# Optimization experiments

Measured on AMD Instinct MI355X. Metric: run time of the kernel, lower is better.

The kernel has to match this reference:

```python
import jax, jax.numpy as jnp
import numpy as np

EPS = 1e-5        # layer_norm_epsilon
N_HEAD = 16
PAD = 50257       # pad_token_id in select_at_last_token
L = 2             # len(layer_nums)


def _ln(x, g, b):
    m = jnp.mean(x, axis=-1, keepdims=True)
    v = jnp.mean(jnp.square(x - m), axis=-1, keepdims=True)
    return (x - m) * jax.lax.rsqrt(v + EPS) * g + b


def _attn_layer(hs, idx, g, b, Wq, Wk, Wv, Wo, bo):
    # hs: [B,S,D]; idx: [B] index of last non-pad token
    B, S, D = hs.shape
    hd = D // N_HEAD
    h = _ln(hs, g, b)
    last = h[jnp.arange(B), idx]                       # [B,D] select_at_last_token
    q = (last @ Wq).reshape(B, N_HEAD, hd)             # single query per sequence
    k = (h @ Wk).reshape(B, S, N_HEAD, hd)
    v = (h @ Wv).reshape(B, S, N_HEAD, hd)
    # GPT-Neo attention: NO 1/sqrt(head_dim) scaling; causal mask for the last
    # row (q_len=1, key_len=S) is all-ones so it is a no-op.
    scores = jnp.einsum('bhd,bshd->bhs', q, k)
    w = jax.nn.softmax(scores, axis=-1)
    o = jnp.einsum('bhs,bshd->bhd', w, v).reshape(B, D)
    return o @ Wo + bo


def setup_inputs() -> dict:
    key = jax.random.key(0)
    ks = jax.random.split(key, 12)
    B, S, D = 8, 2048, 2048
    Dc = L * D            # 4096, MLP input size
    I = 4 * Dc            # 16384, mlp_ratio * Dc
    s = 0.02
    return {
        'hs0': jax.random.normal(ks[0], (B, S, D), jnp.float32),
        'hs1': jax.random.normal(ks[1], (B, S, D), jnp.float32),
        'ids': jax.random.randint(ks[2], (B, S), 0, 50258),
        'ln_g': jnp.ones((L, D), jnp.float32),
        'ln_b': jnp.zeros((L, D), jnp.float32),
        'Wq': jax.random.normal(ks[3], (L, D, D), jnp.float32) * s,
        'Wk': jax.random.normal(ks[4], (L, D, D), jnp.float32) * s,
        'Wv': jax.random.normal(ks[5], (L, D, D), jnp.float32) * s,
        'Wo': jax.random.normal(ks[6], (L, D, D), jnp.float32) * s,
        'bo': jnp.zeros((L, D), jnp.float32),
        'W1': jax.random.normal(ks[7], (Dc, I), jnp.float32) * s,
        'b1': jnp.zeros((I,), jnp.float32),
        'W2': jax.random.normal(ks[8], (I, Dc), jnp.float32) * s,
        'b2': jnp.zeros((Dc,), jnp.float32),
        'Wl': jax.random.normal(ks[9], (Dc, 2), jnp.float32) * s,
        'bl': jnp.zeros((2,), jnp.float32),
    }


def reference(hs0, hs1, ids, ln_g, ln_b, Wq, Wk, Wv, Wo, bo, W1, b1, W2, b2, Wl, bl):
    # select_at_last_token index: argmax of cumsum of non-pad mask = last non-pad pos
    mask = (ids != PAD).astype(jnp.int32)
    idx = jnp.argmax(jnp.cumsum(mask, axis=1), axis=1)  # [B]
    hss = [hs0, hs1]
    attn_outs = [
        _attn_layer(hss[l], idx, ln_g[l], ln_b[l], Wq[l], Wk[l], Wv[l], Wo[l], bo[l])
        for l in range(L)
    ]
    h = jnp.concatenate(attn_outs, axis=-1)            # [B, L*D]
    m = jax.nn.gelu(h @ W1 + b1, approximate=False) @ W2 + b2
    h = h + m                                           # residual around MLP
    return h @ Wl + bl                                  # [B, 2] logits
```

## Files before the change

### kernel.cpp

```cpp
#include <hip/hip_runtime.h>
#include <math.h>

#define PAD_ID 50257
#define B_ 8
#define S_ 2048
#define D_ 2048
#define H_ 16
#define HD_ 128
#define L_ 2
#define DC_ 4096
#define I_ 16384
#define EPS_ 1e-5f

__device__ __forceinline__ int rfl(int x){ return __builtin_amdgcn_readfirstlane(x); }

__global__ __launch_bounds__(256) void kA(const int* __restrict__ ids, int* __restrict__ idx){
  int b = blockIdx.x, t = threadIdx.x;
  __shared__ int red[256];
  int best = -1;
  for (int s = t; s < S_; s += 256)
    if (ids[b*S_+s] != PAD_ID) best = s;
  red[t] = best; __syncthreads();
  for (int off=128; off; off>>=1){ if (t<off) red[t] = max(red[t], red[t+off]); __syncthreads(); }
  if (t==0) idx[b] = max(red[0], 0);
}

__global__ __launch_bounds__(256) void kA2(const float* __restrict__ hs0, const float* __restrict__ hs1,
                    const int* __restrict__ idx,
                    const float* __restrict__ g, const float* __restrict__ bt,
                    float* __restrict__ lnlT){
  int b = blockIdx.x, l = blockIdx.y, t = threadIdx.x;
  const float* hs = (l==0?hs0:hs1);
  const float* row = hs + ((size_t)b*S_ + idx[b])*D_;
  int d0 = t*8;
  float x[8]; float s=0.f, ss=0.f;
  #pragma unroll
  for(int k=0;k<8;k++){ x[k]=row[d0+k]; s+=x[k]; ss+=x[k]*x[k]; }
  __shared__ float r1[256], r2[256];
  r1[t]=s; r2[t]=ss; __syncthreads();
  for(int off=128; off; off>>=1){ if(t<off){ r1[t]+=r1[t+off]; r2[t]+=r2[t+off]; } __syncthreads(); }
  float m = r1[0]*(1.0f/D_); float var = r2[0]*(1.0f/D_) - m*m;
  float rstd = rsqrtf(var + EPS_);
  #pragma unroll
  for(int k=0;k<8;k++){
    int d = d0+k;
    lnlT[((size_t)l*D_ + d)*8 + b] = (x[k]-m)*rstd*g[l*D_+d] + bt[l*D_+d];
  }
}

__global__ __launch_bounds__(256) void gemv8(
    const float* __restrict__ W, const float* __restrict__ Xt, float* __restrict__ outAcc,
    int C, int N, int cs, long wStride, long xStride, long oStride){
  int t = threadIdx.x;
  int l = blockIdx.z;
  W += (size_t)l*wStride; Xt += (size_t)l*xStride; outAcc += (size_t)l*oStride;
  int lane = t & 63;
  int w = rfl(t >> 6);
  int cpw = C/(cs*4);
  int c0 = (blockIdx.y*4 + w)*cpw;
  float acc[8] = {0,0,0,0,0,0,0,0};
  const float* xp = Xt + (size_t)c0*8;
  const float* wp = W + (size_t)c0*N + (size_t)blockIdx.x*64 + lane;
  #pragma unroll 4
  for (int c=0; c<cpw; c++){
    float wv = wp[(size_t)c*N];
    #pragma unroll
    for(int r=0;r<8;r++) acc[r] += xp[c*8+r]*wv;
  }
  __shared__ float red[4][64][8];
  #pragma unroll
  for(int r=0;r<8;r++) red[w][lane][r] = acc[r];
  __syncthreads();
  if (t < 64){
    #pragma unroll
    for(int r=0;r<8;r++){
      float s = red[0][t][r]+red[1][t][r]+red[2][t][r]+red[3][t][r];
      atomicAdd(&outAcc[((size_t)blockIdx.x*64 + t)*8 + r], s);
    }
  }
}

__global__ __launch_bounds__(256) void kC(
    const float* __restrict__ Wk, const float* __restrict__ qT,
    const float* __restrict__ g, const float* __restrict__ bt,
    float* __restrict__ gqk, float* __restrict__ Sg, float* __restrict__ Sb){
  int t = threadIdx.x;
  int dq = blockIdx.x; int h = blockIdx.y; int l = blockIdx.z;
  const float* wkB = Wk + (size_t)l*D_*D_ + h*HD_;
  const float* qB  = qT + ((size_t)l*D_ + h*HD_)*8;
  float sgl[8]={0,0,0,0,0,0,0,0}, sbl[8]={0,0,0,0,0,0,0,0};
  for (int rr=0; rr<2; rr++){
    int dp = dq*512 + rr*256 + t;
    const float* wr = wkB + (size_t)dp*D_;
    float a[8]={0,0,0,0,0,0,0,0};
    #pragma unroll 4
    for (int j=0;j<HD_;j++){
      float wv = wr[j];
      #pragma unroll
      for(int r=0;r<8;r++) a[r] += wv*qB[j*8+r];
    }
    float gg = g[l*D_+dp], bb = bt[l*D_+dp];
    #pragma unroll
    for(int r=0;r<8;r++){
      float gq = gg*a[r];
      gqk[((size_t)(l*8+r)*H_ + h)*D_ + dp] = gq;
      sgl[r] += gq;
      sbl[r] += bb*a[r];
    }
  }
  __shared__ float red[256][8];
  #pragma unroll
  for(int r=0;r<8;r++) red[t][r]=sgl[r];
  __syncthreads();
  for(int off=128; off; off>>=1){ if(t<off){ for(int r=0;r<8;r++) red[t][r]+=red[t+off][r]; } __syncthreads(); }
  if (t<8) atomicAdd(&Sg[(l*8+t)*H_ + h], red[0][t]);
  __syncthreads();
  #pragma unroll
  for(int r=0;r<8;r++) red[t][r]=sbl[r];
  __syncthreads();
  for(int off=128; off; off>>=1){ if(t<off){ for(int r=0;r<8;r++) red[t][r]+=red[t+off][r]; } __syncthreads(); }
  if (t<8) atomicAdd(&Sb[(l*8+t)*H_ + h], red[0][t]);
}

__global__ __launch_bounds__(256) void kD(
    const float* __restrict__ hs0, const float* __restrict__ hs1,
    const float* __restrict__ gqk, const float* __restrict__ Sg, const float* __restrict__ Sb,
    float* __restrict__ scores, float* __restrict__ mu, float* __restrict__ rs){
  int t = threadIdx.x;
  int sc = blockIdx.x, b = blockIdx.y, l = blockIdx.z;
  const float* hs = (l==0?hs0:hs1) + (size_t)b*S_*D_;
  int r = t & 63;
  int jq = rfl(t >> 6);
  int s0 = sc*64;
  __shared__ float lds[64*65];
  float acc[16];
  #pragma unroll
  for(int h=0;h<16;h++) acc[h]=0.f;
  float sum=0.f, sq=0.f;
  const float* gq = gqk + (size_t)(l*8+b)*H_*D_;
  for (int jt=0; jt<32; jt++){
    int jb = jt*64;
    #pragma unroll
    for (int q=0;q<4;q++){
      int fid = t + q*256;
      int row = fid >> 4, jo = (fid & 15)*4;
      const float4 v = *(const float4*)(hs + (size_t)(s0+row)*D_ + jb + jo);
      float* lp = &lds[row*65 + jo];
      lp[0]=v.x; lp[1]=v.y; lp[2]=v.z; lp[3]=v.w;
    }
    __syncthreads();
    #pragma unroll
    for (int jj4=0; jj4<4; jj4++){
      int j = jq*16 + jj4*4;
      float x0 = lds[r*65+j], x1 = lds[r*65+j+1], x2 = lds[r*65+j+2], x3 = lds[r*65+j+3];
      sum += x0+x1+x2+x3;
      sq += x0*x0; sq += x1*x1; sq += x2*x2; sq += x3*x3;
      int jg = jb + j;
      #pragma unroll
      for(int h=0;h<16;h++){
        const float4 gv = *(const float4*)(gq + (size_t)h*D_ + jg);
        acc[h] += x0*gv.x + x1*gv.y + x2*gv.z + x3*gv.w;
      }
    }
    __syncthreads();
  }
  if (jq > 0){
    float* p = &lds[((jq-1)*64 + r)*18];
    #pragma unroll
    for(int h=0;h<16;h++) p[h]=acc[h];
    p[16]=sum; p[17]=sq;
  }
  __syncthreads();
  if (jq == 0){
    #pragma unroll
    for(int g3=0; g3<3; g3++){
      const float* p = &lds[(g3*64 + r)*18];
      #pragma unroll
      for(int h=0;h<16;h++) acc[h]+=p[h];
      sum += p[16]; sq += p[17];
    }
    float m = sum * (1.0f/D_);
    float var = sq * (1.0f/D_) - m*m;
    float rst = rsqrtf(var + EPS_);
    int s = s0 + r;
    int lb = l*8+b;
    mu[(size_t)lb*S_ + s] = m;
    rs[(size_t)lb*S_ + s] = rst;
    #pragma unroll
    for(int h=0;h<16;h++){
      float sgv = Sg[lb*H_ + h], sbv = Sb[lb*H_ + h];
      scores[((size_t)lb*H_ + h)*S_ + s] = rst*(acc[h] - m*sgv) + sbv;
    }
  }
}

__global__ __launch_bounds__(256) void kE1(
    const float* __restrict__ scores, const float* __restrict__ mu, const float* __restrict__ rs,
    float* __restrict__ M, float* __restrict__ Sden, float* __restrict__ cc){
  int t=threadIdx.x; int h=blockIdx.x, b=blockIdx.y, l=blockIdx.z;
  int lb = l*8+b;
  const float* sc = scores + ((size_t)lb*H_ + h)*S_;
  __shared__ float red[256];
  __shared__ float red2[256];
  float mx = -1e30f;
  for (int s=t; s<S_; s+=256) mx = fmaxf(mx, sc[s]);
  red[t]=mx; __syncthreads();
  for(int off=128;off;off>>=1){ if(t<off) red[t]=fmaxf(red[t],red[t+off]); __syncthreads(); }
  float Mv = red[0];
  __syncthreads();
  float se=0.f, sce=0.f;
  const float* mup = mu + (size_t)lb*S_;
  const float* rsp = rs + (size_t)lb*S_;
  for (int s=t; s<S_; s+=256){
    float e = __expf(sc[s]-Mv);
    se += e;
    sce += e*rsp[s]*mup[s];
  }
  red[t]=se; red2[t]=sce; __syncthreads();
  for(int off=128;off;off>>=1){ if(t<off){red[t]+=red[t+off]; red2[t]+=red2[t+off];} __syncthreads(); }
  if(t==0){ M[lb*H_+h]=Mv; Sden[lb*H_+h]=red[0]; cc[lb*H_+h]=red2[0]/red[0]; }
}

__global__ __launch_bounds__(256) void kE2(
    const float* __restrict__ scores, const float* __restrict__ rs,
    const float* __restrict__ M, const float* __restrict__ Sden,
    float* __restrict__ u){
  int t=threadIdx.x; int scb=blockIdx.x, b=blockIdx.y, l=blockIdx.z;
  int lb=l*8+b;
  int lin0 = t*8;
  int sl = lin0 >> 4;
  int h0 = lin0 & 15;
  int s = scb*128 + sl;
  float rstv = rs[(size_t)lb*S_ + s];
  float out[8];
  #pragma unroll
  for(int k=0;k<8;k++){
    int h = h0 + k;
    float e = __expf(scores[((size_t)lb*H_+h)*S_ + s] - M[lb*H_+h]);
    out[k] = e / Sden[lb*H_+h] * rstv;
  }
  float* up = u + ((size_t)lb*S_ + s)*H_ + h0;
  *(float4*)up     = make_float4(out[0],out[1],out[2],out[3]);
  *(float4*)(up+4) = make_float4(out[4],out[5],out[6],out[7]);
}

__global__ __launch_bounds__(256) void kF(
    const float* __restrict__ hs0, const float* __restrict__ hs1,
    const float* __restrict__ u, float* __restrict__ Fpart){
  int t=threadIdx.x;
  int sc = blockIdx.x>>1, dh = blockIdx.x&1;
  int b=blockIdx.y, l=blockIdx.z;
  int lb=l*8+b;
  const float* hs = (l==0?hs0:hs1) + (size_t)b*S_*D_;
  int d0 = dh*1024 + t*4;
  float acc[16][4];
  #pragma unroll
  for(int h=0;h<16;h++){
    #pragma unroll
    for(int k=0;k<4;k++) acc[h][k]=0.f;
  }
  int s0 = sc*128;
  for (int si=0; si<128; si++){
    int s = s0+si;
    const float* up = u + ((size_t)lb*S_ + s)*H_;
    float4 u0 = *(const float4*)up, u1 = *(const float4*)(up+4),
           u2 = *(const float4*)(up+8), u3 = *(const float4*)(up+12);
    float uu[16] = {u0.x,u0.y,u0.z,u0.w, u1.x,u1.y,u1.z,u1.w,
                    u2.x,u2.y,u2.z,u2.w, u3.x,u3.y,u3.z,u3.w};
    float4 x = *(const float4*)(hs + (size_t)s*D_ + d0);
    float xx[4]={x.x,x.y,x.z,x.w};
    #pragma unroll
    for(int h=0;h<16;h++){
      #pragma unroll
      for(int k=0;k<4;k++) acc[h][k] += uu[h]*xx[k];
    }
  }
  #pragma unroll
  for(int h=0;h<16;h++){
    float4 v = make_float4(acc[h][0],acc[h][1],acc[h][2],acc[h][3]);
    *(float4*)(Fpart + (((size_t)lb*16 + sc)*H_ + h)*D_ + d0) = v;
  }
}

__global__ __launch_bounds__(256) void kF2(
    const float* __restrict__ Fpart, const float* __restrict__ g, float* __restrict__ gAT){
  int n = blockIdx.x*256 + threadIdx.x;
  int d = n & (D_-1);
  int h = (n >> 11) & 15;
  int l = n >> 15;
  float gg = g[l*D_+d];
  float out[8];
  #pragma unroll
  for(int b=0;b<8;b++){
    float s=0.f;
    for(int scn=0;scn<16;scn++)
      s += Fpart[(((size_t)(l*8+b)*16 + scn)*H_ + h)*D_ + d];
    out[b]=gg*s;
  }
  float* op = gAT + (size_t)n*8;
  *(float4*)op     = make_float4(out[0],out[1],out[2],out[3]);
  *(float4*)(op+4) = make_float4(out[4],out[5],out[6],out[7]);
}

__global__ __launch_bounds__(256) void kG(
    const float* __restrict__ Wv, const float* __restrict__ gAT,
    const float* __restrict__ g, const float* __restrict__ bt,
    float* __restrict__ Opart){
  int t=threadIdx.x;
  int d4=blockIdx.x, h=blockIdx.y, l=blockIdx.z;
  int j = t & 127;
  int dg = rfl(t >> 7);
  const float* wv = Wv + (size_t)l*D_*D_ + h*HD_ + j;
  const float* gA = gAT + ((size_t)l*H_ + h)*D_*8;
  float acc[8]={0,0,0,0,0,0,0,0}; float ag=0.f, ab=0.f;
  int dstart = d4*512 + dg*256;
  #pragma unroll 2
  for (int dd=0; dd<256; dd++){
    int d = dstart+dd;
    float wvv = wv[(size_t)d*D_];
    const float* xa = gA + (size_t)d*8;
    #pragma unroll
    for(int r=0;r<8;r++) acc[r] += xa[r]*wvv;
    ag += g[l*D_+d]*wvv;
    ab += bt[l*D_+d]*wvv;
  }
  __shared__ float red[2][128][10];
  float* p = red[dg][j];
  #pragma unroll
  for(int r=0;r<8;r++) p[r]=acc[r];
  p[8]=ag; p[9]=ab;
  __syncthreads();
  if (t<128){
    const float* q0=red[0][t]; const float* q1=red[1][t];
    #pragma unroll
    for(int r=0;r<10;r++)
      atomicAdd(&Opart[(((size_t)l*H_+h)*HD_ + t)*10 + r], q0[r]+q1[r]);
  }
}

__global__ __launch_bounds__(256) void kG2(const float* __restrict__ Opart, const float* __restrict__ cc,
                    float* __restrict__ oT){
  int n = blockIdx.x*256 + threadIdx.x;
  int j = n & 127; int h = (n>>7) & 15; int l = n>>11;
  const float* p = Opart + (size_t)n*10;
  float ag=p[8], ab=p[9];
  #pragma unroll
  for(int b=0;b<8;b++){
    float c = cc[(l*8+b)*H_+h];
    oT[((size_t)l*D_ + h*HD_ + j)*8 + b] = p[b] - c*ag + ab;
  }
}

__global__ void kInitH(const float* __restrict__ bo, float* __restrict__ hcatT){
  int n = blockIdx.x*256 + threadIdx.x;
  hcatT[n] = bo[n>>3];
}

__global__ void kH2(float* __restrict__ t1T, const float* __restrict__ b1){
  int i = blockIdx.x*256 + threadIdx.x;
  float bv = b1[i];
  float* p = t1T + (size_t)i*8;
  #pragma unroll
  for(int k=0;k<8;k++){
    float x = p[k] + bv;
    p[k] = 0.5f*x*(1.0f + erff(x*0.70710678118654752440f));
  }
}

__global__ void kH2b(const float* __restrict__ hcatT, const float* __restrict__ b2, float* __restrict__ h2T){
  int j = blockIdx.x*256 + threadIdx.x;
  float bv = b2[j];
  #pragma unroll
  for(int k=0;k<8;k++) h2T[(size_t)j*8+k] = hcatT[(size_t)j*8+k] + bv;
}

__global__ __launch_bounds__(256) void kH4(const float* __restrict__ h2T, const float* __restrict__ Wl,
                    const float* __restrict__ bl, float* __restrict__ out){
  int t=threadIdx.x;
  float acc[8][2];
  #pragma unroll
  for(int b=0;b<8;b++){acc[b][0]=0.f;acc[b][1]=0.f;}
  for (int j=t; j<DC_; j+=256){
    float w0=Wl[j*2], w1=Wl[j*2+1];
    const float* hp = h2T + (size_t)j*8;
    #pragma unroll
    for(int b=0;b<8;b++){ float x=hp[b]; acc[b][0]+=x*w0; acc[b][1]+=x*w1; }
  }
  __shared__ float red[256][16];
  #pragma unroll
  for(int b=0;b<8;b++){ red[t][b*2]=acc[b][0]; red[t][b*2+1]=acc[b][1]; }
  __syncthreads();
  for(int off=128;off;off>>=1){ if(t<off){ for(int k=0;k<16;k++) red[t][k]+=red[t+off][k]; } __syncthreads(); }
  if (t<16) out[t] = red[0][t] + bl[t&1];
}

extern "C" void kernel_launch(void* const* d_in, const int* in_sizes, int n_in,
                              void* d_out, int out_size, void* d_ws, size_t ws_size,
                              hipStream_t stream) {
  (void)in_sizes; (void)n_in; (void)out_size;
  const float* hs0 = (const float*)d_in[0];
  const float* hs1 = (const float*)d_in[1];
  const int*   ids = (const int*)d_in[2];
  const float* ln_g = (const float*)d_in[3];
  const float* ln_b = (const float*)d_in[4];
  const float* Wq = (const float*)d_in[5];
  const float* Wk = (const float*)d_in[6];
  const float* Wv = (const float*)d_in[7];
  const float* Wo = (const float*)d_in[8];
  const float* bo = (const float*)d_in[9];
  const float* W1 = (const float*)d_in[10];
  const float* b1 = (const float*)d_in[11];
  const float* W2 = (const float*)d_in[12];
  const float* b2 = (const float*)d_in[13];
  const float* Wl = (const float*)d_in[14];
  const float* bl = (const float*)d_in[15];
  float* out = (float*)d_out;
  float* ws = (float*)d_ws;

  size_t o = 0;
  int* idx = (int*)ws;        o += 16;
  float* qT = ws + o;         o += (size_t)L_*D_*8;
  float* Sg = ws + o;         o += 256;
  float* Sb = ws + o;         o += 256;
  float* Opart = ws + o;      o += (size_t)L_*H_*HD_*10;
  float* t1T = ws + o;        o += (size_t)I_*8;
  size_t atomicFloats = o - 16;
  float* lnlT = ws + o;       o += (size_t)L_*D_*8;
  float* gqk = ws + o;        o += (size_t)L_*8*H_*D_;
  float* mu = ws + o;         o += (size_t)L_*8*S_;
  float* rs_ = ws + o;        o += (size_t)L_*8*S_;
  float* scores = ws + o;     o += (size_t)L_*8*H_*S_;
  float* M = ws + o;          o += 256;
  float* Sden = ws + o;       o += 256;
  float* cc = ws + o;         o += 256;
  float* u = ws + o;          o += (size_t)L_*8*S_*H_;
  float* Fpart = ws + o;      o += (size_t)L_*8*16*H_*D_;
  float* gAT = ws + o;        o += (size_t)L_*H_*D_*8;
  float* oT = ws + o;         o += (size_t)L_*D_*8;
  float* hcatT = ws + o;      o += (size_t)DC_*8;
  float* h2T = ws + o;        o += (size_t)DC_*8;
  if (o*4 > ws_size) return;

  hipMemsetAsync((void*)(ws + 16), 0, atomicFloats*4, stream);

  kA<<<8,256,0,stream>>>(ids, idx);
  kA2<<<dim3(8,2),256,0,stream>>>(hs0,hs1,idx,ln_g,ln_b,lnlT);
  gemv8<<<dim3(32,2,2),256,0,stream>>>(Wq, lnlT, qT, D_, D_, 2,
                                       (long)D_*D_, (long)D_*8, (long)D_*8);
  kC<<<dim3(4,16,2),256,0,stream>>>(Wk, qT, ln_g, ln_b, gqk, Sg, Sb);
  kD<<<dim3(32,8,2),256,0,stream>>>(hs0,hs1,gqk,Sg,Sb,scores,mu,rs_);
  kE1<<<dim3(16,8,2),256,0,stream>>>(scores,mu,rs_,M,Sden,cc);
  kE2<<<dim3(16,8,2),256,0,stream>>>(scores,rs_,M,Sden,u);
  kF<<<dim3(32,8,2),256,0,stream>>>(hs0,hs1,u,Fpart);
  kF2<<<256,256,0,stream>>>(Fpart, ln_g, gAT);
  kG<<<dim3(4,16,2),256,0,stream>>>(Wv, gAT, ln_g, ln_b, Opart);
  kG2<<<16,256,0,stream>>>(Opart, cc, oT);
  kInitH<<<128,256,0,stream>>>(bo, hcatT);
  gemv8<<<dim3(32,2,2),256,0,stream>>>(Wo, oT, hcatT, D_, D_, 2,
                                       (long)D_*D_, (long)D_*8, (long)D_*8);
  gemv8<<<dim3(256,2,1),256,0,stream>>>(W1, hcatT, t1T, DC_, I_, 2, 0,0,0);
  kH2<<<64,256,0,stream>>>(t1T, b1);
  kH2b<<<16,256,0,stream>>>(hcatT, b2, h2T);
  gemv8<<<dim3(64,8,1),256,0,stream>>>(W2, t1T, h2T, I_, DC_, 8, 0,0,0);
  kH4<<<1,256,0,stream>>>(h2T, Wl, bl, out);
}
```

Measured before the change: 1.134 ms.

## Retile score kernel with LDS-staged gqk, split-K, and widen grids across kernels

The score kernel kD now stages both hs and the gqk tile in LDS and uses a 4-row by 4-column register tile per thread. It splits the D reduction into two halves, then adds a new kD2 kernel that sums the partials and applies the LayerNorm correction. kC, kF, kG and the gemv8 launches are re-split into more blocks with smaller per-thread work to raise parallelism. The change adds an extra kernel launch and a partial-buffer round trip, and it reuses the Fpart workspace for the kD partials.

```diff
diff --git a/kernel.cpp b/kernel.cpp
--- a/kernel.cpp
+++ b/kernel.cpp
@@ -85,28 +85,27 @@
     const float* __restrict__ g, const float* __restrict__ bt,
     float* __restrict__ gqk, float* __restrict__ Sg, float* __restrict__ Sb){
   int t = threadIdx.x;
-  int dq = blockIdx.x; int h = blockIdx.y; int l = blockIdx.z;
-  const float* wkB = Wk + (size_t)l*D_*D_ + h*HD_;
-  const float* qB  = qT + ((size_t)l*D_ + h*HD_)*8;
-  float sgl[8]={0,0,0,0,0,0,0,0}, sbl[8]={0,0,0,0,0,0,0,0};
-  for (int rr=0; rr<2; rr++){
-    int dp = dq*512 + rr*256 + t;
-    const float* wr = wkB + (size_t)dp*D_;
-    float a[8]={0,0,0,0,0,0,0,0};
-    #pragma unroll 4
-    for (int j=0;j<HD_;j++){
-      float wv = wr[j];
-      #pragma unroll
-      for(int r=0;r<8;r++) a[r] += wv*qB[j*8+r];
-    }
-    float gg = g[l*D_+dp], bb = bt[l*D_+dp];
-    #pragma unroll
-    for(int r=0;r<8;r++){
-      float gq = gg*a[r];
-      gqk[((size_t)(l*8+r)*H_ + h)*D_ + dp] = gq;
-      sgl[r] += gq;
-      sbl[r] += bb*a[r];
-    }
+  int h = blockIdx.y; int l = blockIdx.z;
+  int dp = blockIdx.x*256 + t;
+  const float* wr = Wk + (size_t)l*D_*D_ + (size_t)dp*D_ + h*HD_;
+  const float* qB = qT + ((size_t)l*D_ + h*HD_)*8;
+  float a[8]={0,0,0,0,0,0,0,0};
+  #pragma unroll 4
+  for (int j4=0;j4<32;j4++){
+    float4 wv = *(const float4*)(wr + j4*4);
+    const float* qp = qB + j4*32;
+    #pragma unroll
+    for(int r=0;r<8;r++)
+      a[r] += wv.x*qp[r] + wv.y*qp[8+r] + wv.z*qp[16+r] + wv.w*qp[24+r];
+  }
+  float gg = g[l*D_+dp], bb = bt[l*D_+dp];
+  float sgl[8], sbl[8];
+  #pragma unroll
+  for(int r=0;r<8;r++){
+    float gq = gg*a[r];
+    gqk[((size_t)(l*8+r)*H_ + h)*D_ + dp] = gq;
+    sgl[r] = gq;
+    sbl[r] = bb*a[r];
   }
   __shared__ float red[256][8];
   #pragma unroll
@@ -124,73 +123,132 @@
 
 __global__ __launch_bounds__(256) void kD(
     const float* __restrict__ hs0, const float* __restrict__ hs1,
-    const float* __restrict__ gqk, const float* __restrict__ Sg, const float* __restrict__ Sb,
-    float* __restrict__ scores, float* __restrict__ mu, float* __restrict__ rs){
+    const float* __restrict__ gqk,
+    float* __restrict__ accP, float* __restrict__ sumP, float* __restrict__ sqP){
   int t = threadIdx.x;
-  int sc = blockIdx.x, b = blockIdx.y, l = blockIdx.z;
+  int sc = blockIdx.x & 31, kh = blockIdx.x >> 5;
+  int b = blockIdx.y, l = blockIdx.z;
+  int lb = l*8 + b;
   const float* hs = (l==0?hs0:hs1) + (size_t)b*S_*D_;
-  int r = t & 63;
-  int jq = rfl(t >> 6);
+  const float* gqp = gqk + (size_t)lb*H_*D_;
   int s0 = sc*64;
-  __shared__ float lds[64*65];
-  float acc[16];
-  #pragma unroll
-  for(int h=0;h<16;h++) acc[h]=0.f;
-  float sum=0.f, sq=0.f;
-  const float* gq = gqk + (size_t)(l*8+b)*H_*D_;
-  for (int jt=0; jt<32; jt++){
-    int jb = jt*64;
+  int kb = kh*1024;
+  __shared__ float smem[64*66 + 16*68];
+  float* xT = smem;
+  float* gT = smem + 64*66;
+  int rq = t & 15, jg = t >> 4;
+  int r0 = rq*4, jc = jg*4;
+  float acc[4][16];
+  #pragma unroll
+  for(int rr=0;rr<4;rr++){
+    #pragma unroll
+    for(int h=0;h<16;h++) acc[rr][h]=0.f;
+  }
+  float sum[4]={0.f,0.f,0.f,0.f}, sq[4]={0.f,0.f,0.f,0.f};
+  for (int c=0;c<16;c++){
+    int cb = kb + c*64;
     #pragma unroll
     for (int q=0;q<4;q++){
       int fid = t + q*256;
       int row = fid >> 4, jo = (fid & 15)*4;
-      const float4 v = *(const float4*)(hs + (size_t)(s0+row)*D_ + jb + jo);
-      float* lp = &lds[row*65 + jo];
-      lp[0]=v.x; lp[1]=v.y; lp[2]=v.z; lp[3]=v.w;
+      float4 v = *(const float4*)(hs + (size_t)(s0+row)*D_ + cb + jo);
+      float2* wp = (float2*)&xT[row*66 + jo];
+      wp[0] = make_float2(v.x, v.y);
+      wp[1] = make_float2(v.z, v.w);
+    }
+    {
+      int hh = t >> 4, jo = (t & 15)*4;
+      float4 gv = *(const float4*)(gqp + (size_t)hh*D_ + cb + jo);
+      *(float4*)&gT[hh*68 + jo] = gv;
     }
     __syncthreads();
-    #pragma unroll
-    for (int jj4=0; jj4<4; jj4++){
-      int j = jq*16 + jj4*4;
-      float x0 = lds[r*65+j], x1 = lds[r*65+j+1], x2 = lds[r*65+j+2], x3 = lds[r*65+j+3];
-      sum += x0+x1+x2+x3;
-      sq += x0*x0; sq += x1*x1; sq += x2*x2; sq += x3*x3;
-      int jg = jb + j;
+    float xv[4][4];
+    #pragma unroll
+    for (int rr=0;rr<4;rr++){
+      const float2* xp = (const float2*)&xT[(r0+rr)*66 + jc];
+      float2 xa = xp[0], xb = xp[1];
+      xv[rr][0]=xa.x; xv[rr][1]=xa.y; xv[rr][2]=xb.x; xv[rr][3]=xb.y;
+      sum[rr] += xa.x + xa.y + xb.x + xb.y;
+      sq[rr]  += xa.x*xa.x + xa.y*xa.y + xb.x*xb.x + xb.y*xb.y;
+    }
+    #pragma unroll
+    for (int h=0;h<16;h++){
+      float4 gv = *(const float4*)&gT[h*68 + jc];
       #pragma unroll
-      for(int h=0;h<16;h++){
-        const float4 gv = *(const float4*)(gq + (size_t)h*D_ + jg);
-        acc[h] += x0*gv.x + x1*gv.y + x2*gv.z + x3*gv.w;
-      }
+      for (int rr=0;rr<4;rr++)
+        acc[rr][h] += xv[rr][0]*gv.x + xv[rr][1]*gv.y + xv[rr][2]*gv.z + xv[rr][3]*gv.w;
     }
     __syncthreads();
   }
-  if (jq > 0){
-    float* p = &lds[((jq-1)*64 + r)*18];
-    #pragma unroll
-    for(int h=0;h<16;h++) p[h]=acc[h];
-    p[16]=sum; p[17]=sq;
-  }
-  __syncthreads();
-  if (jq == 0){
-    #pragma unroll
-    for(int g3=0; g3<3; g3++){
-      const float* p = &lds[(g3*64 + r)*18];
+  #pragma unroll
+  for (int rr=0;rr<4;rr++){
+    #pragma unroll
+    for (int h=0;h<16;h++){
+      float v = acc[rr][h];
+      v += __shfl_xor(v, 16);
+      v += __shfl_xor(v, 32);
+      acc[rr][h] = v;
+    }
+    float sv = sum[rr]; sv += __shfl_xor(sv, 16); sv += __shfl_xor(sv, 32); sum[rr] = sv;
+    float qv = sq[rr];  qv += __shfl_xor(qv, 16); qv += __shfl_xor(qv, 32); sq[rr]  = qv;
+  }
+  __syncthreads();
+  float* redL = smem;
+  int w = t >> 6;
+  if ((t & 63) < 16){
+    float* p = &redL[(w*16 + rq)*73];
+    #pragma unroll
+    for (int rr=0;rr<4;rr++){
       #pragma unroll
-      for(int h=0;h<16;h++) acc[h]+=p[h];
-      sum += p[16]; sq += p[17];
-    }
-    float m = sum * (1.0f/D_);
-    float var = sq * (1.0f/D_) - m*m;
-    float rst = rsqrtf(var + EPS_);
-    int s = s0 + r;
-    int lb = l*8+b;
-    mu[(size_t)lb*S_ + s] = m;
-    rs[(size_t)lb*S_ + s] = rst;
-    #pragma unroll
-    for(int h=0;h<16;h++){
-      float sgv = Sg[lb*H_ + h], sbv = Sb[lb*H_ + h];
-      scores[((size_t)lb*H_ + h)*S_ + s] = rst*(acc[h] - m*sgv) + sbv;
-    }
+      for (int h=0;h<16;h++) p[rr*16+h] = acc[rr][h];
+      p[64+rr] = sum[rr];
+      p[68+rr] = sq[rr];
+    }
+  }
+  __syncthreads();
+  if (t < 64){
+    int frq = t >> 2, frr = t & 3;
+    float ah[16];
+    #pragma unroll
+    for(int h=0;h<16;h++) ah[h]=0.f;
+    float s1=0.f, s2=0.f;
+    #pragma unroll
+    for (int ww=0; ww<4; ww++){
+      const float* p = &redL[(ww*16 + frq)*73];
+      #pragma unroll
+      for(int h=0;h<16;h++) ah[h] += p[frr*16+h];
+      s1 += p[64+frr];
+      s2 += p[68+frr];
+    }
+    int s = s0 + t;
+    size_t base = (size_t)(kh*16 + lb)*16;
+    #pragma unroll
+    for(int h=0;h<16;h++)
+      accP[(base + h)*S_ + s] = ah[h];
+    sumP[(size_t)(kh*16+lb)*S_ + s] = s1;
+    sqP[(size_t)(kh*16+lb)*S_ + s] = s2;
+  }
+}
+
+__global__ __launch_bounds__(256) void kD2(
+    const float* __restrict__ accP, const float* __restrict__ sumP, const float* __restrict__ sqP,
+    const float* __restrict__ Sg, const float* __restrict__ Sb,
+    float* __restrict__ scores, float* __restrict__ mu, float* __restrict__ rs){
+  int t = threadIdx.x;
+  int b = blockIdx.y, l = blockIdx.z;
+  int lb = l*8 + b;
+  int s = blockIdx.x*256 + t;
+  float s1 = sumP[(size_t)lb*S_ + s] + sumP[(size_t)(16+lb)*S_ + s];
+  float s2 = sqP[(size_t)lb*S_ + s]  + sqP[(size_t)(16+lb)*S_ + s];
+  float m = s1*(1.0f/D_);
+  float var = s2*(1.0f/D_) - m*m;
+  float rst = rsqrtf(var + EPS_);
+  mu[(size_t)lb*S_ + s] = m;
+  rs[(size_t)lb*S_ + s] = rst;
+  #pragma unroll
+  for (int h=0;h<16;h++){
+    float a = accP[((size_t)lb*16 + h)*S_ + s] + accP[((size_t)(16+lb)*16 + h)*S_ + s];
+    scores[((size_t)lb*H_ + h)*S_ + s] = rst*(a - m*Sg[lb*H_+h]) + Sb[lb*H_+h];
   }
 }
 
@@ -248,18 +306,16 @@
     const float* __restrict__ hs0, const float* __restrict__ hs1,
     const float* __restrict__ u, float* __restrict__ Fpart){
   int t=threadIdx.x;
-  int sc = blockIdx.x>>1, dh = blockIdx.x&1;
+  int sc = blockIdx.x>>2, dq = blockIdx.x&3;
   int b=blockIdx.y, l=blockIdx.z;
   int lb=l*8+b;
   const float* hs = (l==0?hs0:hs1) + (size_t)b*S_*D_;
-  int d0 = dh*1024 + t*4;
-  float acc[16][4];
-  #pragma unroll
-  for(int h=0;h<16;h++){
-    #pragma unroll
-    for(int k=0;k<4;k++) acc[h][k]=0.f;
-  }
+  int d0 = dq*512 + t*2;
+  float acc[16][2];
+  #pragma unroll
+  for(int h=0;h<16;h++){ acc[h][0]=0.f; acc[h][1]=0.f; }
   int s0 = sc*128;
+  #pragma unroll 4
   for (int si=0; si<128; si++){
     int s = s0+si;
     const float* up = u + ((size_t)lb*S_ + s)*H_;
@@ -267,19 +323,13 @@
            u2 = *(const float4*)(up+8), u3 = *(const float4*)(up+12);
     float uu[16] = {u0.x,u0.y,u0.z,u0.w, u1.x,u1.y,u1.z,u1.w,
                     u2.x,u2.y,u2.z,u2.w, u3.x,u3.y,u3.z,u3.w};
-    float4 x = *(const float4*)(hs + (size_t)s*D_ + d0);
-    float xx[4]={x.x,x.y,x.z,x.w};
-    #pragma unroll
-    for(int h=0;h<16;h++){
-      #pragma unroll
-      for(int k=0;k<4;k++) acc[h][k] += uu[h]*xx[k];
-    }
-  }
-  #pragma unroll
-  for(int h=0;h<16;h++){
-    float4 v = make_float4(acc[h][0],acc[h][1],acc[h][2],acc[h][3]);
-    *(float4*)(Fpart + (((size_t)lb*16 + sc)*H_ + h)*D_ + d0) = v;
-  }
+    float2 x = *(const float2*)(hs + (size_t)s*D_ + d0);
+    #pragma unroll
+    for(int h=0;h<16;h++){ acc[h][0] += uu[h]*x.x; acc[h][1] += uu[h]*x.y; }
+  }
+  #pragma unroll
+  for(int h=0;h<16;h++)
+    *(float2*)(Fpart + (((size_t)lb*16 + sc)*H_ + h)*D_ + d0) = make_float2(acc[h][0], acc[h][1]);
 }
 
 __global__ __launch_bounds__(256) void kF2(
@@ -313,9 +363,9 @@
   const float* wv = Wv + (size_t)l*D_*D_ + h*HD_ + j;
   const float* gA = gAT + ((size_t)l*H_ + h)*D_*8;
   float acc[8]={0,0,0,0,0,0,0,0}; float ag=0.f, ab=0.f;
-  int dstart = d4*512 + dg*256;
+  int dstart = d4*256 + dg*128;
   #pragma unroll 2
-  for (int dd=0; dd<256; dd++){
+  for (int dd=0; dd<128; dd++){
     int d = dstart+dd;
     float wvv = wv[(size_t)d*D_];
     const float* xa = gA + (size_t)d*8;
@@ -338,7 +388,7 @@
   }
 }
 
-__global__ __launch_bounds__(256) void kG2(const float* __restrict__ Opart, const float* __restrict__ cc,
+__global__ void kG2(const float* __restrict__ Opart, const float* __restrict__ cc,
                     float* __restrict__ oT){
   int n = blockIdx.x*256 + threadIdx.x;
   int j = n & 127; int h = (n>>7) & 15; int l = n>>11;
@@ -441,26 +491,31 @@
   float* h2T = ws + o;        o += (size_t)DC_*8;
   if (o*4 > ws_size) return;
 
+  float* accP = Fpart;
+  float* sumP = Fpart + (size_t)2*16*16*2048;
+  float* sqP  = sumP + (size_t)2*16*2048;
+
   hipMemsetAsync((void*)(ws + 16), 0, atomicFloats*4, stream);
 
   kA<<<8,256,0,stream>>>(ids, idx);
   kA2<<<dim3(8,2),256,0,stream>>>(hs0,hs1,idx,ln_g,ln_b,lnlT);
-  gemv8<<<dim3(32,2,2),256,0,stream>>>(Wq, lnlT, qT, D_, D_, 2,
+  gemv8<<<dim3(32,8,2),256,0,stream>>>(Wq, lnlT, qT, D_, D_, 8,
                                        (long)D_*D_, (long)D_*8, (long)D_*8);
-  kC<<<dim3(4,16,2),256,0,stream>>>(Wk, qT, ln_g, ln_b, gqk, Sg, Sb);
-  kD<<<dim3(32,8,2),256,0,stream>>>(hs0,hs1,gqk,Sg,Sb,scores,mu,rs_);
+  kC<<<dim3(8,16,2),256,0,stream>>>(Wk, qT, ln_g, ln_b, gqk, Sg, Sb);
+  kD<<<dim3(64,8,2),256,0,stream>>>(hs0,hs1,gqk,accP,sumP,sqP);
+  kD2<<<dim3(8,8,2),256,0,stream>>>(accP,sumP,sqP,Sg,Sb,scores,mu,rs_);
   kE1<<<dim3(16,8,2),256,0,stream>>>(scores,mu,rs_,M,Sden,cc);
   kE2<<<dim3(16,8,2),256,0,stream>>>(scores,rs_,M,Sden,u);
-  kF<<<dim3(32,8,2),256,0,stream>>>(hs0,hs1,u,Fpart);
+  kF<<<dim3(64,8,2),256,0,stream>>>(hs0,hs1,u,Fpart);
   kF2<<<256,256,0,stream>>>(Fpart, ln_g, gAT);
-  kG<<<dim3(4,16,2),256,0,stream>>>(Wv, gAT, ln_g, ln_b, Opart);
+  kG<<<dim3(8,16,2),256,0,stream>>>(Wv, gAT, ln_g, ln_b, Opart);
   kG2<<<16,256,0,stream>>>(Opart, cc, oT);
   kInitH<<<128,256,0,stream>>>(bo, hcatT);
-  gemv8<<<dim3(32,2,2),256,0,stream>>>(Wo, oT, hcatT, D_, D_, 2,
+  gemv8<<<dim3(32,8,2),256,0,stream>>>(Wo, oT, hcatT, D_, D_, 8,
                                        (long)D_*D_, (long)D_*8, (long)D_*8);
-  gemv8<<<dim3(256,2,1),256,0,stream>>>(W1, hcatT, t1T, DC_, I_, 2, 0,0,0);
+  gemv8<<<dim3(256,4,1),256,0,stream>>>(W1, hcatT, t1T, DC_, I_, 4, 0,0,0);
   kH2<<<64,256,0,stream>>>(t1T, b1);
   kH2b<<<16,256,0,stream>>>(hcatT, b2, h2T);
-  gemv8<<<dim3(64,8,1),256,0,stream>>>(W2, t1T, h2T, I_, DC_, 8, 0,0,0);
+  gemv8<<<dim3(64,16,1),256,0,stream>>>(W2, t1T, h2T, I_, DC_, 16, 0,0,0);
   kH4<<<1,256,0,stream>>>(h2T, Wl, bl, out);
 }
```

New measurement: 1.016 ms. 1.12x faster.
